# Kernel optimization log

Hardware: AMD Instinct MI355X
Metric: run time of the kernel (lower is better)

Reference implementation:

```python
import jax, jax.numpy as jnp
import numpy as np

H = 16
K = 64

def setup_inputs() -> dict:
    key = jax.random.key(0)
    k1, k2, k3 = jax.random.split(key, 3)
    b, m, d = 8, 1024, 1024
    x = jax.random.normal(k1, (b, m, d), dtype=jnp.float32)
    P_i = jax.random.normal(k2, (d, 3 * d), dtype=jnp.float32) * (1.0 / np.sqrt(d))
    P_o = jax.random.normal(k3, (d, d), dtype=jnp.float32) * (1.0 / np.sqrt(d))
    return {"x": x, "P_i": P_i, "P_o": P_o}

def reference(x, P_i, P_o):
    b, m, d = x.shape
    # fused QKV projection: [b, m, 3d] -> [b, m, h, 3k] -> [b, h, m, 3k]
    t = (x @ P_i).reshape(b, m, H, 3 * K).transpose(0, 2, 1, 3)
    Q, Kt, V = t[..., :K], t[..., K:2 * K], t[..., 2 * K:]
    logits = jnp.einsum('bhmk,bhnk->bhmn', Q, Kt) / jnp.sqrt(jnp.float32(K))
    # causal mask (tril): position m attends to n <= m
    causal = jnp.tril(jnp.ones((m, m), dtype=bool))
    logits = jnp.where(causal[None, None], logits, jnp.float32(-jnp.inf))
    w = jax.nn.softmax(logits, axis=-1)
    o = jnp.einsum('bhmn,bhnk->bhmk', w, V)  # [b, h, m, k]
    y = o.transpose(0, 2, 1, 3).reshape(b, m, H * K) @ P_o
    return y
```

## Files before the change

kernel.cpp:

```cpp
#include <hip/hip_runtime.h>

typedef unsigned short u16;
typedef __bf16 b16x8_t __attribute__((ext_vector_type(8)));
typedef unsigned short u16x8 __attribute__((ext_vector_type(8)));
typedef float f32x4 __attribute__((ext_vector_type(4)));

__device__ __forceinline__ u16 f2bf(float f) {
  union { float f; unsigned u; } x; x.f = f;
  unsigned r = x.u + 0x7fffu + ((x.u >> 16) & 1u);
  return (u16)(r >> 16);
}

__device__ __forceinline__ f32x4 mfma16(u16x8 a, u16x8 b, f32x4 c) {
  return __builtin_amdgcn_mfma_f32_16x16x32_bf16(
      __builtin_bit_cast(b16x8_t, a), __builtin_bit_cast(b16x8_t, b), c, 0, 0, 0);
}

__device__ __forceinline__ void gld_lds16(const void* g, void* l) {
  __builtin_amdgcn_global_load_lds(
      (const __attribute__((address_space(1))) void*)g,
      (__attribute__((address_space(3))) void*)l, 16, 0, 0);
}

__device__ __forceinline__ void store_out(float* p, float v) { *p = v; }
__device__ __forceinline__ void store_out(u16* p, float v) { *p = f2bf(v); }

__global__ __launch_bounds__(256) void prep(const float* __restrict__ x,
                                            u16* __restrict__ xbf,
                                            const float* __restrict__ Pi,
                                            u16* __restrict__ piT,
                                            const float* __restrict__ Po,
                                            u16* __restrict__ poT) {
  __shared__ float t[32][33];
  const int bid = blockIdx.x, tid = threadIdx.x;
  if (bid < 8192) {
    int i = bid * 256 + tid;
    float4 f = ((const float4*)x)[i];
    u16 a0 = f2bf(f.x), a1 = f2bf(f.y), a2 = f2bf(f.z), a3 = f2bf(f.w);
    unsigned lo = (unsigned)a0 | ((unsigned)a1 << 16);
    unsigned hi = (unsigned)a2 | ((unsigned)a3 << 16);
    ((uint2*)xbf)[i] = make_uint2(lo, hi);
    return;
  }
  const float* src; u16* dst; int R, Cn, bx, by;
  if (bid < 11264) {
    int tb = bid - 8192;  src = Pi; dst = piT; R = 1024; Cn = 3072;
    bx = tb % 96; by = tb / 96;
  } else {
    int tb = bid - 11264; src = Po; dst = poT; R = 1024; Cn = 1024;
    bx = tb % 32; by = tb / 32;
  }
  const int tx = tid & 31, ty = tid >> 5;
  const int c0 = bx * 32, r0 = by * 32;
  for (int j = 0; j < 32; j += 8)
    t[ty + j][tx] = src[(size_t)(r0 + ty + j) * Cn + c0 + tx];
  __syncthreads();
  for (int j = 0; j < 32; j += 8)
    dst[(size_t)(c0 + ty + j) * R + r0 + tx] = f2bf(t[tx][ty + j]);
}

template <typename OutT, int BN, int EPI>
__global__ __launch_bounds__(256, 2) void gemm_v7(const u16* __restrict__ A,
                                                  const u16* __restrict__ Bt,
                                                  OutT* __restrict__ C,
                                                  u16* __restrict__ Vt,
                                                  int M, int N, int K) {
  constexpr int NB = BN / 64;
  constexpr int NJ = BN / 32;
  constexpr int NL = 2 + NB;
  __shared__ __align__(16) u16 sA[3][4096];
  __shared__ __align__(16) u16 sB[3][BN * 32];
  const int tid = threadIdx.x, lane = tid & 63, wid = tid >> 6;
  const int hi = lane >> 4, ln = lane & 15;
  const int wm = (wid >> 1) * 64, wn = (wid & 1) * (BN / 2);

  const int gdx = gridDim.x;
  const int nwg = gdx * gridDim.y;
  int wg = blockIdx.y * gdx + blockIdx.x;
  wg = (wg & 7) * (nwg >> 3) + (wg >> 3);
  const int m0 = (wg / gdx) * 128;
  const int n0 = (wg % gdx) * BN;

  const int sr = tid >> 2;
  const int scsw = ((tid & 3) ^ ((tid >> 3) & 3)) * 8;
  const u16* srcA = A + (size_t)(m0 + sr) * K + scsw;
  const u16* srcB = Bt + (size_t)(n0 + sr) * K + scsw;
  const size_t K64 = (size_t)64 * K;

  auto stage = [&](int buf, int t) {
    const int k0 = t * 32;
    gld_lds16(srcA + k0, &sA[buf][tid * 8]);
    gld_lds16(srcA + K64 + k0, &sA[buf][2048 + tid * 8]);
    gld_lds16(srcB + k0, &sB[buf][tid * 8]);
    gld_lds16(srcB + K64 + k0, &sB[buf][2048 + tid * 8]);
    if (NB > 2) gld_lds16(srcB + 2 * K64 + k0, &sB[buf][4096 + tid * 8]);
  };

  const int csw = (hi ^ ((ln >> 1) & 3)) * 8;
  int offA[4], offB[NJ];
#pragma unroll
  for (int i = 0; i < 4; ++i) offA[i] = (wm + i * 16 + ln) * 32 + csw;
#pragma unroll
  for (int j = 0; j < NJ; ++j) offB[j] = (wn + j * 16 + ln) * 32 + csw;

  f32x4 acc[4][NJ] = {};
  const int NT = K >> 5;

  stage(0, 0); stage(1, 1);
  if constexpr (NL == 5) asm volatile("s_waitcnt vmcnt(5)" ::: "memory");
  else                   asm volatile("s_waitcnt vmcnt(4)" ::: "memory");
  __builtin_amdgcn_s_barrier();

  int cb = 0, sb = 2;
  for (int kt = 0; kt < NT; ++kt) {
    u16x8 af[4], bf[NJ];
#pragma unroll
    for (int i = 0; i < 4; ++i) af[i] = *(const u16x8*)(&sA[cb][offA[i]]);
#pragma unroll
    for (int j = 0; j < NJ; ++j) bf[j] = *(const u16x8*)(&sB[cb][offB[j]]);
    if (kt + 2 < NT) {
      stage(sb, kt + 2);
      sb = (sb == 2) ? 0 : sb + 1;
      if constexpr (NL == 5) asm volatile("s_waitcnt vmcnt(5)" ::: "memory");
      else                   asm volatile("s_waitcnt vmcnt(4)" ::: "memory");
    } else {
      asm volatile("s_waitcnt vmcnt(0)" ::: "memory");
    }
    __builtin_amdgcn_s_barrier();
    asm volatile("s_waitcnt lgkmcnt(0)" ::: "memory");
    __builtin_amdgcn_sched_barrier(0);
    __builtin_amdgcn_s_setprio(1);
#pragma unroll
    for (int i = 0; i < 4; ++i)
#pragma unroll
      for (int j = 0; j < NJ; ++j)
        acc[i][j] = mfma16(af[i], bf[j], acc[i][j]);
    __builtin_amdgcn_s_setprio(0);
    __builtin_amdgcn_sched_barrier(0);
    __builtin_amdgcn_s_barrier();
    cb = (cb == 2) ? 0 : cb + 1;
  }

#pragma unroll
  for (int i = 0; i < 4; ++i) {
    int rr = m0 + wm + i * 16 + hi * 4;
#pragma unroll
    for (int j = 0; j < NJ; ++j) {
      int colw = wn + j * 16 + ln;
      if (EPI == 1 && colw >= 128) {
        int h = n0 / 192, kk = colw - 128;
        int b = rr >> 10, n = rr & 1023;
        ushort4 pk;
        pk.x = f2bf(acc[i][j][0]); pk.y = f2bf(acc[i][j][1]);
        pk.z = f2bf(acc[i][j][2]); pk.w = f2bf(acc[i][j][3]);
        *(ushort4*)(Vt + ((size_t)(b * 16 + h) * 64 + kk) * 1024 + n) = pk;
      } else {
        float sc = (EPI == 1 && colw < 64) ? 0.125f : 1.f;
        int col = n0 + colw;
#pragma unroll
        for (int r = 0; r < 4; ++r)
          store_out(&C[(size_t)(rr + r) * N + col], acc[i][j][r] * sc);
      }
    }
  }
}

__global__ __launch_bounds__(512, 4) void attn_fwd7(const u16* __restrict__ QKV,
                                                    const u16* __restrict__ Vt,
                                                    u16* __restrict__ O) {
  __shared__ __align__(16) u16 sK[2][4096];
  __shared__ __align__(16) u16 sVt[2][4096];
  __shared__ __align__(16) u16 sP[8][16 * 72];
  const int tid = threadIdx.x, lane = tid & 63, wid = tid >> 6;
  const int bid = blockIdx.x;
  const int w = (bid & 7) * 64 + (bid >> 3);
  const int z = w & 3, h = (w >> 2) & 15, bb = w >> 6;
  const size_t rowbase = (size_t)bb * 1024;
  const size_t vbase = ((size_t)bb * 16 + h) * 64;
  const int colQ = h * 192, colK = colQ + 64;
  const int hi = lane >> 4, ln = lane & 15;
  const int slr = lane >> 3;
  const int sle = ((lane & 7) ^ slr) * 8;
  u16* sPw = sP[wid];
  const u16x8 onesf = {0x3F80, 0x3F80, 0x3F80, 0x3F80, 0x3F80, 0x3F80, 0x3F80, 0x3F80};

  auto stageKV = [&](int buf, int nt) {
    const int n0g = nt * 64;
    gld_lds16(QKV + (rowbase + n0g + 8 * wid + slr) * 3072 + colK + sle,
              &sK[buf][wid * 512]);
    gld_lds16(Vt + (vbase + 8 * wid + slr) * 1024 + n0g + sle,
              &sVt[buf][wid * 512]);
  };

  const int mtA = z, mtB = 7 - z;
  const int qrow0A = mtA * 128 + wid * 16;
  const int qrow0B = mtB * 128 + wid * 16;
  const int ntA = 2 * mtA + 2, ntB = 2 * mtB + 2;

  u16x8 qfA[2], qfB[2];
#pragma unroll
  for (int kb = 0; kb < 2; ++kb) {
    qfA[kb] = *(const u16x8*)(QKV + (rowbase + qrow0A + ln) * 3072 + colQ + kb * 32 + hi * 8);
    qfB[kb] = *(const u16x8*)(QKV + (rowbase + qrow0B + ln) * 3072 + colQ + kb * 32 + hi * 8);
  }

  f32x4 oA[4] = {}, oB[4] = {};
  f32x4 laccA = {0.f, 0.f, 0.f, 0.f}, laccB = {0.f, 0.f, 0.f, 0.f};

  auto computeHalf = [&](const u16x8* qf, f32x4* o, f32x4& lacc, int qrow0,
                         int buf, int n0g) {
    f32x4 s[4] = {};
    __builtin_amdgcn_s_setprio(1);
#pragma unroll
    for (int kb = 0; kb < 2; ++kb)
#pragma unroll
      for (int j = 0; j < 4; ++j) {
        int row = j * 16 + ln;
        int cb = (kb * 64 + hi * 16) ^ ((row & 7) << 4);
        u16x8 kfr = *(const u16x8*)(&sK[buf][(row * 128 + cb) >> 1]);
        s[j] = mfma16(qf[kb], kfr, s[j]);
      }
    __builtin_amdgcn_s_setprio(0);
    if (n0g + 63 > qrow0) {
#pragma unroll
      for (int j = 0; j < 4; ++j) {
        int col = n0g + j * 16 + ln;
#pragma unroll
        for (int r = 0; r < 4; ++r)
          if (col > qrow0 + hi * 4 + r) s[j][r] = -3e38f;
      }
    }
#pragma unroll
    for (int j = 0; j < 4; ++j)
#pragma unroll
      for (int r = 0; r < 4; ++r)
        sPw[(hi * 4 + r) * 72 + j * 16 + ln] = f2bf(__expf(s[j][r]));
    u16x8 pf[2];
#pragma unroll
    for (int kb2 = 0; kb2 < 2; ++kb2)
      pf[kb2] = *(const u16x8*)(&sPw[ln * 72 + kb2 * 32 + hi * 8]);
    __builtin_amdgcn_s_setprio(1);
    lacc = mfma16(pf[0], onesf, lacc);
    lacc = mfma16(pf[1], onesf, lacc);
#pragma unroll
    for (int dt = 0; dt < 4; ++dt)
#pragma unroll
      for (int kb2 = 0; kb2 < 2; ++kb2) {
        int row = dt * 16 + ln;
        int cb = (kb2 * 64 + hi * 16) ^ ((row & 7) << 4);
        u16x8 vfr = *(const u16x8*)(&sVt[buf][(row * 128 + cb) >> 1]);
        o[dt] = mfma16(pf[kb2], vfr, o[dt]);
      }
    __builtin_amdgcn_s_setprio(0);
  };

  stageKV(0, 0);
  for (int nt = 0; nt < ntB; ++nt) {
    __syncthreads();
    if (nt + 1 < ntB) stageKV((nt + 1) & 1, nt + 1);
    const int buf = nt & 1;
    const int n0g = nt * 64;
    if (nt < ntA && n0g <= qrow0A + 15) computeHalf(qfA, oA, laccA, qrow0A, buf, n0g);
    if (n0g <= qrow0B + 15)             computeHalf(qfB, oB, laccB, qrow0B, buf, n0g);
  }

#pragma unroll
  for (int r = 0; r < 4; ++r) {
    float invA = 1.f / laccA[r];
    float invB = 1.f / laccB[r];
#pragma unroll
    for (int dt = 0; dt < 4; ++dt) {
      O[(rowbase + qrow0A + hi * 4 + r) * 1024 + h * 64 + dt * 16 + ln] =
          f2bf(oA[dt][r] * invA);
      O[(rowbase + qrow0B + hi * 4 + r) * 1024 + h * 64 + dt * 16 + ln] =
          f2bf(oB[dt][r] * invB);
    }
  }
}

extern "C" void kernel_launch(void* const* d_in, const int* in_sizes, int n_in,
                              void* d_out, int out_size, void* d_ws, size_t ws_size,
                              hipStream_t stream) {
  const float* x = (const float*)d_in[0];
  const float* Pi = (const float*)d_in[1];
  const float* Po = (const float*)d_in[2];
  float* y = (float*)d_out;
  char* ws = (char*)d_ws;

  u16* qkv  = (u16*)(ws);
  u16* piT  = (u16*)(ws + 50331648);
  u16* poT  = (u16*)(ws + 56623104);
  u16* xbf  = (u16*)(ws + 58720256);
  u16* vt   = (u16*)(ws + 75497472);
  u16* obuf = (u16*)(ws + 58720256);

  prep<<<12288, 256, 0, stream>>>(x, xbf, Pi, piT, Po, poT);

  gemm_v7<u16, 192, 1><<<dim3(16, 64), 256, 0, stream>>>(xbf, piT, qkv, vt,
                                                         8192, 3072, 1024);
  attn_fwd7<<<512, 512, 0, stream>>>(qkv, vt, obuf);
  gemm_v7<float, 128, 0><<<dim3(8, 64), 256, 0, stream>>>(obuf, poT, y, nullptr,
                                                          8192, 1024, 1024);
}
```

Before: 132.9 us.

## Use 32x32x16 MFMA in a dedicated QKV projection GEMM kernel

Adds a new gemm32 kernel for the QKV projection that uses the 32x32x16 bf16 MFMA instruction instead of 16x16x32, with new LDS fragment offsets and a matching epilogue for the Q scaling and V transpose. The larger MFMA shape is meant to cut LDS fragment reads per FLOP and raise matrix-core throughput. The gemm_v7 epilogue is simplified because its EPI=1 V path is no longer used. The 32x32 accumulator layout makes the C stores more scattered, and the larger accumulators may raise register pressure.

```diff
diff --git a/kernel.cpp b/kernel.cpp
--- a/kernel.cpp
+++ b/kernel.cpp
@@ -4,6 +4,7 @@
 typedef __bf16 b16x8_t __attribute__((ext_vector_type(8)));
 typedef unsigned short u16x8 __attribute__((ext_vector_type(8)));
 typedef float f32x4 __attribute__((ext_vector_type(4)));
+typedef float f32x16 __attribute__((ext_vector_type(16)));
 
 __device__ __forceinline__ u16 f2bf(float f) {
   union { float f; unsigned u; } x; x.f = f;
@@ -13,6 +14,11 @@
 
 __device__ __forceinline__ f32x4 mfma16(u16x8 a, u16x8 b, f32x4 c) {
   return __builtin_amdgcn_mfma_f32_16x16x32_bf16(
+      __builtin_bit_cast(b16x8_t, a), __builtin_bit_cast(b16x8_t, b), c, 0, 0, 0);
+}
+
+__device__ __forceinline__ f32x16 mfma32(u16x8 a, u16x8 b, f32x16 c) {
+  return __builtin_amdgcn_mfma_f32_32x32x16_bf16(
       __builtin_bit_cast(b16x8_t, a), __builtin_bit_cast(b16x8_t, b), c, 0, 0, 0);
 }
 
@@ -59,6 +65,130 @@
     dst[(size_t)(c0 + ty + j) * R + r0 + tx] = f2bf(t[tx][ty + j]);
 }
 
+__global__ __launch_bounds__(256, 2) void gemm32(const u16* __restrict__ A,
+                                                 const u16* __restrict__ Bt,
+                                                 u16* __restrict__ C,
+                                                 u16* __restrict__ Vt,
+                                                 int M, int N, int K) {
+  __shared__ __align__(16) u16 sA[3][4096];
+  __shared__ __align__(16) u16 sB[3][6144];
+  const int tid = threadIdx.x, lane = tid & 63, wid = tid >> 6;
+  const int l31 = lane & 31, l5 = lane >> 5;
+  const int wm = (wid >> 1) * 64, wn = (wid & 1) * 96;
+
+  const int gdx = gridDim.x;
+  const int nwg = gdx * gridDim.y;
+  int wg = blockIdx.y * gdx + blockIdx.x;
+  wg = (wg & 7) * (nwg >> 3) + (wg >> 3);
+  const int m0 = (wg / gdx) * 128;
+  const int n0 = (wg % gdx) * 192;
+
+  const int sr = tid >> 2;
+  const int scsw = ((tid & 3) ^ ((tid >> 3) & 3)) * 8;
+  const u16* srcA = A + (size_t)(m0 + sr) * K + scsw;
+  const u16* srcB = Bt + (size_t)(n0 + sr) * K + scsw;
+  const size_t K64 = (size_t)64 * K;
+
+  auto stage = [&](int buf, int t) {
+    const int k0 = t * 32;
+    gld_lds16(srcA + k0, &sA[buf][tid * 8]);
+    gld_lds16(srcA + K64 + k0, &sA[buf][2048 + tid * 8]);
+    gld_lds16(srcB + k0, &sB[buf][tid * 8]);
+    gld_lds16(srcB + K64 + k0, &sB[buf][2048 + tid * 8]);
+    gld_lds16(srcB + 2 * K64 + k0, &sB[buf][4096 + tid * 8]);
+  };
+
+  const int sw = (l31 >> 1) & 3;
+  int offA32[2][2], offB32[3][2];
+#pragma unroll
+  for (int mt = 0; mt < 2; ++mt)
+#pragma unroll
+    for (int kh = 0; kh < 2; ++kh)
+      offA32[mt][kh] = (wm + mt * 32 + l31) * 32 + (((kh * 2 + l5) ^ sw) * 8);
+#pragma unroll
+  for (int nt = 0; nt < 3; ++nt)
+#pragma unroll
+    for (int kh = 0; kh < 2; ++kh)
+      offB32[nt][kh] = (wn + nt * 32 + l31) * 32 + (((kh * 2 + l5) ^ sw) * 8);
+
+  f32x16 acc[2][3] = {};
+  const int NT = K >> 5;
+
+  stage(0, 0); stage(1, 1);
+  asm volatile("s_waitcnt vmcnt(5)" ::: "memory");
+  __builtin_amdgcn_s_barrier();
+
+  int cb = 0, sb = 2;
+  for (int kt = 0; kt < NT; ++kt) {
+    u16x8 af[2][2], bf[3][2];
+#pragma unroll
+    for (int mt = 0; mt < 2; ++mt)
+#pragma unroll
+      for (int kh = 0; kh < 2; ++kh)
+        af[mt][kh] = *(const u16x8*)(&sA[cb][offA32[mt][kh]]);
+#pragma unroll
+    for (int nt = 0; nt < 3; ++nt)
+#pragma unroll
+      for (int kh = 0; kh < 2; ++kh)
+        bf[nt][kh] = *(const u16x8*)(&sB[cb][offB32[nt][kh]]);
+    if (kt + 2 < NT) {
+      stage(sb, kt + 2);
+      sb = (sb == 2) ? 0 : sb + 1;
+      asm volatile("s_waitcnt vmcnt(5)" ::: "memory");
+    } else {
+      asm volatile("s_waitcnt vmcnt(0)" ::: "memory");
+    }
+    __builtin_amdgcn_s_barrier();
+    asm volatile("s_waitcnt lgkmcnt(0)" ::: "memory");
+    __builtin_amdgcn_sched_barrier(0);
+    __builtin_amdgcn_s_setprio(1);
+#pragma unroll
+    for (int kh = 0; kh < 2; ++kh)
+#pragma unroll
+      for (int mt = 0; mt < 2; ++mt)
+#pragma unroll
+        for (int nt = 0; nt < 3; ++nt)
+          acc[mt][nt] = mfma32(af[mt][kh], bf[nt][kh], acc[mt][nt]);
+    __builtin_amdgcn_s_setprio(0);
+    __builtin_amdgcn_sched_barrier(0);
+    __builtin_amdgcn_s_barrier();
+    cb = (cb == 2) ? 0 : cb + 1;
+  }
+
+#pragma unroll
+  for (int mt = 0; mt < 2; ++mt) {
+    const int rbase = m0 + wm + mt * 32 + 4 * l5;
+#pragma unroll
+    for (int nt = 0; nt < 3; ++nt) {
+      int colw = wn + nt * 32 + l31;
+      if (colw >= 128) {
+        int h = n0 / 192, kk = colw - 128;
+#pragma unroll
+        for (int g = 0; g < 4; ++g) {
+          int row = rbase + 8 * g;
+          int b = row >> 10, n = row & 1023;
+          ushort4 pk;
+          pk.x = f2bf(acc[mt][nt][4 * g + 0]);
+          pk.y = f2bf(acc[mt][nt][4 * g + 1]);
+          pk.z = f2bf(acc[mt][nt][4 * g + 2]);
+          pk.w = f2bf(acc[mt][nt][4 * g + 3]);
+          *(ushort4*)(Vt + ((size_t)(b * 16 + h) * 64 + kk) * 1024 + n) = pk;
+        }
+      } else {
+        float sc = (colw < 64) ? 0.125f : 1.f;
+        int col = n0 + colw;
+#pragma unroll
+        for (int g = 0; g < 4; ++g)
+#pragma unroll
+          for (int r2 = 0; r2 < 4; ++r2) {
+            int row = rbase + 8 * g + r2;
+            C[(size_t)row * N + col] = f2bf(acc[mt][nt][4 * g + r2] * sc);
+          }
+      }
+    }
+  }
+}
+
 template <typename OutT, int BN, int EPI>
 __global__ __launch_bounds__(256, 2) void gemm_v7(const u16* __restrict__ A,
                                                   const u16* __restrict__ Bt,
@@ -147,20 +277,11 @@
 #pragma unroll
     for (int j = 0; j < NJ; ++j) {
       int colw = wn + j * 16 + ln;
-      if (EPI == 1 && colw >= 128) {
-        int h = n0 / 192, kk = colw - 128;
-        int b = rr >> 10, n = rr & 1023;
-        ushort4 pk;
-        pk.x = f2bf(acc[i][j][0]); pk.y = f2bf(acc[i][j][1]);
-        pk.z = f2bf(acc[i][j][2]); pk.w = f2bf(acc[i][j][3]);
-        *(ushort4*)(Vt + ((size_t)(b * 16 + h) * 64 + kk) * 1024 + n) = pk;
-      } else {
-        float sc = (EPI == 1 && colw < 64) ? 0.125f : 1.f;
-        int col = n0 + colw;
-#pragma unroll
-        for (int r = 0; r < 4; ++r)
-          store_out(&C[(size_t)(rr + r) * N + col], acc[i][j][r] * sc);
-      }
+      float sc = (EPI == 1 && colw < 64) ? 0.125f : 1.f;
+      int col = n0 + colw;
+#pragma unroll
+      for (int r = 0; r < 4; ++r)
+        store_out(&C[(size_t)(rr + r) * N + col], acc[i][j][r] * sc);
     }
   }
 }
@@ -296,8 +417,7 @@
 
   prep<<<12288, 256, 0, stream>>>(x, xbf, Pi, piT, Po, poT);
 
-  gemm_v7<u16, 192, 1><<<dim3(16, 64), 256, 0, stream>>>(xbf, piT, qkv, vt,
-                                                         8192, 3072, 1024);
+  gemm32<<<dim3(16, 64), 256, 0, stream>>>(xbf, piT, qkv, vt, 8192, 3072, 1024);
   attn_fwd7<<<512, 512, 0, stream>>>(qkv, vt, obuf);
   gemm_v7<float, 128, 0><<<dim3(8, 64), 256, 0, stream>>>(obuf, poT, y, nullptr,
                                                           8192, 1024, 1024);
```

Result: slower. 140.6 us (+5.8%).

## Switch GEMM to BK=64 double-buffered pipeline with 8-way LDS swizzle

Applied to the files above, without the earlier changes.

Restructures the projection GEMMs from a triple-buffered BK=32 pipeline to a double-buffered BK=64 pipeline. Each k-tile now does two MFMA sub-steps, which halves the barrier count per K, and the XOR swizzle widens to 8 chunks to fit 64-element rows. In exchange, prefetch depth drops to one tile, there is a full vmcnt(0) wait every iteration, and dropping the occupancy hint of 2 blocks per SM may change register allocation.

```diff
diff --git a/kernel.cpp b/kernel.cpp
--- a/kernel.cpp
+++ b/kernel.cpp
@@ -60,16 +60,15 @@
 }
 
 template <typename OutT, int BN, int EPI>
-__global__ __launch_bounds__(256, 2) void gemm_v7(const u16* __restrict__ A,
-                                                  const u16* __restrict__ Bt,
-                                                  OutT* __restrict__ C,
-                                                  u16* __restrict__ Vt,
-                                                  int M, int N, int K) {
-  constexpr int NB = BN / 64;
+__global__ __launch_bounds__(256) void gemm_bk64(const u16* __restrict__ A,
+                                                 const u16* __restrict__ Bt,
+                                                 OutT* __restrict__ C,
+                                                 u16* __restrict__ Vt,
+                                                 int M, int N, int K) {
   constexpr int NJ = BN / 32;
-  constexpr int NL = 2 + NB;
-  __shared__ __align__(16) u16 sA[3][4096];
-  __shared__ __align__(16) u16 sB[3][BN * 32];
+  constexpr int NGB = BN / 32;
+  __shared__ __align__(16) u16 sA[2][8192];
+  __shared__ __align__(16) u16 sB[2][BN * 64];
   const int tid = threadIdx.x, lane = tid & 63, wid = tid >> 6;
   const int hi = lane >> 4, ln = lane & 15;
   const int wm = (wid >> 1) * 64, wn = (wid & 1) * (BN / 2);
@@ -81,64 +80,68 @@
   const int m0 = (wg / gdx) * 128;
   const int n0 = (wg % gdx) * BN;
 
-  const int sr = tid >> 2;
-  const int scsw = ((tid & 3) ^ ((tid >> 3) & 3)) * 8;
-  const u16* srcA = A + (size_t)(m0 + sr) * K + scsw;
-  const u16* srcB = Bt + (size_t)(n0 + sr) * K + scsw;
-  const size_t K64 = (size_t)64 * K;
+  const int sr = tid >> 3;
+  const int ssw = ((tid & 7) ^ (sr & 7)) * 8;
+  const u16* srcA = A + (size_t)(m0 + sr) * K + ssw;
+  const u16* srcB = Bt + (size_t)(n0 + sr) * K + ssw;
+  const size_t K32 = (size_t)32 * K;
 
   auto stage = [&](int buf, int t) {
-    const int k0 = t * 32;
-    gld_lds16(srcA + k0, &sA[buf][tid * 8]);
-    gld_lds16(srcA + K64 + k0, &sA[buf][2048 + tid * 8]);
-    gld_lds16(srcB + k0, &sB[buf][tid * 8]);
-    gld_lds16(srcB + K64 + k0, &sB[buf][2048 + tid * 8]);
-    if (NB > 2) gld_lds16(srcB + 2 * K64 + k0, &sB[buf][4096 + tid * 8]);
+    const int k0 = t * 64;
+#pragma unroll
+    for (int g = 0; g < 4; ++g)
+      gld_lds16(srcA + (size_t)g * K32 + k0, &sA[buf][g * 2048 + tid * 8]);
+#pragma unroll
+    for (int g = 0; g < NGB; ++g)
+      gld_lds16(srcB + (size_t)g * K32 + k0, &sB[buf][g * 2048 + tid * 8]);
   };
 
-  const int csw = (hi ^ ((ln >> 1) & 3)) * 8;
-  int offA[4], offB[NJ];
-#pragma unroll
-  for (int i = 0; i < 4; ++i) offA[i] = (wm + i * 16 + ln) * 32 + csw;
-#pragma unroll
-  for (int j = 0; j < NJ; ++j) offB[j] = (wn + j * 16 + ln) * 32 + csw;
+  int offA[4][2], offB[NJ][2];
+#pragma unroll
+  for (int i = 0; i < 4; ++i) {
+    int row = wm + i * 16 + ln;
+#pragma unroll
+    for (int s = 0; s < 2; ++s)
+      offA[i][s] = row * 64 + (((s * 4 + hi) ^ (ln & 7)) * 8);
+  }
+#pragma unroll
+  for (int j = 0; j < NJ; ++j) {
+    int row = wn + j * 16 + ln;
+#pragma unroll
+    for (int s = 0; s < 2; ++s)
+      offB[j][s] = row * 64 + (((s * 4 + hi) ^ (ln & 7)) * 8);
+  }
 
   f32x4 acc[4][NJ] = {};
-  const int NT = K >> 5;
-
-  stage(0, 0); stage(1, 1);
-  if constexpr (NL == 5) asm volatile("s_waitcnt vmcnt(5)" ::: "memory");
-  else                   asm volatile("s_waitcnt vmcnt(4)" ::: "memory");
+  const int NT = K >> 6;
+
+  stage(0, 0);
+  asm volatile("s_waitcnt vmcnt(0)" ::: "memory");
   __builtin_amdgcn_s_barrier();
 
-  int cb = 0, sb = 2;
   for (int kt = 0; kt < NT; ++kt) {
-    u16x8 af[4], bf[NJ];
-#pragma unroll
-    for (int i = 0; i < 4; ++i) af[i] = *(const u16x8*)(&sA[cb][offA[i]]);
-#pragma unroll
-    for (int j = 0; j < NJ; ++j) bf[j] = *(const u16x8*)(&sB[cb][offB[j]]);
-    if (kt + 2 < NT) {
-      stage(sb, kt + 2);
-      sb = (sb == 2) ? 0 : sb + 1;
-      if constexpr (NL == 5) asm volatile("s_waitcnt vmcnt(5)" ::: "memory");
-      else                   asm volatile("s_waitcnt vmcnt(4)" ::: "memory");
-    } else {
-      asm volatile("s_waitcnt vmcnt(0)" ::: "memory");
+    const int cb = kt & 1;
+    if (kt + 1 < NT) stage(cb ^ 1, kt + 1);
+#pragma unroll
+    for (int s = 0; s < 2; ++s) {
+      u16x8 af[4], bf[NJ];
+#pragma unroll
+      for (int i = 0; i < 4; ++i) af[i] = *(const u16x8*)(&sA[cb][offA[i][s]]);
+#pragma unroll
+      for (int j = 0; j < NJ; ++j) bf[j] = *(const u16x8*)(&sB[cb][offB[j][s]]);
+      asm volatile("s_waitcnt lgkmcnt(0)" ::: "memory");
+      __builtin_amdgcn_sched_barrier(0);
+      __builtin_amdgcn_s_setprio(1);
+#pragma unroll
+      for (int i = 0; i < 4; ++i)
+#pragma unroll
+        for (int j = 0; j < NJ; ++j)
+          acc[i][j] = mfma16(af[i], bf[j], acc[i][j]);
+      __builtin_amdgcn_s_setprio(0);
+      __builtin_amdgcn_sched_barrier(0);
     }
+    asm volatile("s_waitcnt vmcnt(0)" ::: "memory");
     __builtin_amdgcn_s_barrier();
-    asm volatile("s_waitcnt lgkmcnt(0)" ::: "memory");
-    __builtin_amdgcn_sched_barrier(0);
-    __builtin_amdgcn_s_setprio(1);
-#pragma unroll
-    for (int i = 0; i < 4; ++i)
-#pragma unroll
-      for (int j = 0; j < NJ; ++j)
-        acc[i][j] = mfma16(af[i], bf[j], acc[i][j]);
-    __builtin_amdgcn_s_setprio(0);
-    __builtin_amdgcn_sched_barrier(0);
-    __builtin_amdgcn_s_barrier();
-    cb = (cb == 2) ? 0 : cb + 1;
   }
 
 #pragma unroll
@@ -296,9 +299,9 @@
 
   prep<<<12288, 256, 0, stream>>>(x, xbf, Pi, piT, Po, poT);
 
-  gemm_v7<u16, 192, 1><<<dim3(16, 64), 256, 0, stream>>>(xbf, piT, qkv, vt,
-                                                         8192, 3072, 1024);
+  gemm_bk64<u16, 192, 1><<<dim3(16, 64), 256, 0, stream>>>(xbf, piT, qkv, vt,
+                                                           8192, 3072, 1024);
   attn_fwd7<<<512, 512, 0, stream>>>(qkv, vt, obuf);
-  gemm_v7<float, 128, 0><<<dim3(8, 64), 256, 0, stream>>>(obuf, poT, y, nullptr,
-                                                          8192, 1024, 1024);
-}
+  gemm_bk64<float, 128, 0><<<dim3(8, 64), 256, 0, stream>>>(obuf, poT, y, nullptr,
+                                                            8192, 1024, 1024);
+}
```

Result: faster. 128.5 us (median of 2 runs) (-3.3%).
